# Optimization experiments

Hardware: AMD Instinct MI355X
Metric: run time of the kernel (lower is better)

The kernel has to match this reference:

```python
import jax, jax.numpy as jnp
import numpy as np

B, H, W, C = 4, 64, 64, 128  # input feature map; num_heads == filters == C


def setup_inputs() -> dict:
    key = jax.random.key(0)
    ks = jax.random.split(key, 5)
    x = jax.random.normal(ks[0], (B, H, W, C), dtype=jnp.float32)
    scale = 0.02  # keep QK^T logits in a sane range for softmax
    Wf = jax.random.normal(ks[1], (C, C), dtype=jnp.float32) * scale
    Wg = jax.random.normal(ks[2], (C, C), dtype=jnp.float32) * scale
    Wh = jax.random.normal(ks[3], (C, C), dtype=jnp.float32) * scale
    Wv = jax.random.normal(ks[4], (C, C), dtype=jnp.float32) * scale
    zeros = jnp.zeros((C,), dtype=jnp.float32)
    return {
        "x": x,
        "Wf": Wf, "bf": zeros,
        "Wg": Wg, "bg": zeros,
        "Wh": Wh, "bh": zeros,
        "Wv": Wv, "bv": zeros,
        "gamma": jnp.float32(0.01),
    }


def reference(x, Wf, bf, Wg, bg, Wh, bh, Wv, bv, gamma):
    b, h, w, c = x.shape
    n = h * w
    xf = x.reshape(b, n, c)  # 1x1 conv == per-pixel linear
    f = xf @ Wf + bf  # [b, n, heads]
    g = xf @ Wg + bg
    v = xf @ Wh + bh
    # full spatial self-attention, unscaled logits (as in the original)
    s = jnp.einsum("bnc,bmc->bnm", f, g)  # [b, n, n]
    att = jax.nn.softmax(s, axis=-1)
    ctx = jnp.einsum("bnm,bmc->bnc", att, v)  # [b, n, heads]
    ctx = gamma * ctx
    # 1x1 conv v (linear activation) + residual
    o = ctx @ Wv + bv + xf
    return o.reshape(b, h, w, -1)
```

## Files before the change

kernel.cpp:

```cpp
#include <hip/hip_runtime.h>
#include <hip/hip_bf16.h>


typedef __hip_bfloat16 bf16;
typedef float  floatx4 __attribute__((ext_vector_type(4)));
typedef short  shortx8 __attribute__((ext_vector_type(8)));
typedef short  shortx4 __attribute__((ext_vector_type(4)));

#define CDIM 128
#define NROW 16384
#define NPB  4096
#define LDW  136
#define LDK  72
#define NSPLIT 4
#define KT   16
#define QTILE 128

__device__ __forceinline__ short f2bf(float v) {
    union { __hip_bfloat16 h; short s; } u; u.h = __float2bfloat16(v); return u.s;
}
__device__ __forceinline__ float bf2f(short s) {
    union { short s2; __hip_bfloat16 h; } u; u.s2 = s; return __bfloat162float(u.h);
}

__global__ __launch_bounds__(256) void proj3_kernel(
    const float* __restrict__ x,
    const float* __restrict__ Wf, const float* __restrict__ bf_,
    const float* __restrict__ Wg, const float* __restrict__ bg_,
    const float* __restrict__ Wh, const float* __restrict__ bh_,
    bf16* __restrict__ f, bf16* __restrict__ g, bf16* __restrict__ vT)
{
    __shared__ bf16 wt[128 * LDW];

    const int t    = threadIdx.x;
    const int wave = t >> 6, lane = t & 63;
    const int quad = lane >> 4, l16 = lane & 15;
    const int mtx    = blockIdx.x >> 8;
    const int rowblk = (blockIdx.x & 255) * 64;
    const int row    = rowblk + wave * 16 + l16;

    const float* Ws[3] = {Wf, Wg, Wh};
    const float* Bs[3] = {bf_, bg_, bh_};
    const float* W    = Ws[mtx];
    const float* bias = Bs[mtx];

    for (int i = t; i < 128 * 32; i += 256) {
        int k = i >> 5, n0 = (i & 31) * 4;
        floatx4 wv = *(const floatx4*)(W + k * CDIM + n0);
#pragma unroll
        for (int j = 0; j < 4; ++j)
            *(short*)&wt[(n0 + j) * LDW + k] = f2bf(wv[j]);
    }

    shortx8 afr[4];
    {
        const float* xp = x + (size_t)row * CDIM + quad * 8;
#pragma unroll
        for (int kc = 0; kc < 4; ++kc) {
            floatx4 u = *(const floatx4*)(xp + kc * 32);
            floatx4 w = *(const floatx4*)(xp + kc * 32 + 4);
            shortx8 a;
            a[0]=f2bf(u[0]); a[1]=f2bf(u[1]); a[2]=f2bf(u[2]); a[3]=f2bf(u[3]);
            a[4]=f2bf(w[0]); a[5]=f2bf(w[1]); a[6]=f2bf(w[2]); a[7]=f2bf(w[3]);
            afr[kc] = a;
        }
    }
    __syncthreads();

    floatx4 acc[8];
#pragma unroll
    for (int nt = 0; nt < 8; ++nt) acc[nt] = (floatx4){0.f, 0.f, 0.f, 0.f};
#pragma unroll
    for (int nt = 0; nt < 8; ++nt) {
        const bf16* wrow = &wt[(nt * 16 + l16) * LDW + quad * 8];
#pragma unroll
        for (int kc = 0; kc < 4; ++kc) {
            shortx8 b = *(const shortx8*)(wrow + kc * 32);
            acc[nt] = __builtin_amdgcn_mfma_f32_16x16x32_bf16(afr[kc], b, acc[nt], 0, 0, 0);
        }
    }

    if (mtx < 2) {
        bf16* dst = (mtx == 0) ? f : g;
#pragma unroll
        for (int nt = 0; nt < 8; ++nt) {
            int col = nt * 16 + l16;
            float bv_ = bias[col];
#pragma unroll
            for (int r = 0; r < 4; ++r) {
                int orow = rowblk + wave * 16 + quad * 4 + r;
                *(short*)&dst[(size_t)orow * CDIM + col] = f2bf(acc[nt][r] + bv_);
            }
        }
    } else {
        __syncthreads();
        bf16* vt = wt;
        const int nloc0 = wave * 16 + quad * 4;
#pragma unroll
        for (int nt = 0; nt < 8; ++nt) {
            int ch = nt * 16 + l16;
            float bv_ = bias[ch];
            shortx4 pk;
#pragma unroll
            for (int r = 0; r < 4; ++r) pk[r] = f2bf(acc[nt][r] + bv_);
            *(shortx4*)&vt[ch * LDK + nloc0] = pk;
        }
        __syncthreads();
        const int ch  = t >> 1;
        const int seg = (t & 1) * 32;
        const int batch = rowblk >> 12;
        const int n0 = (rowblk & 4095) + seg;
        bf16* dst = &vT[((size_t)batch * CDIM + ch) * NPB + n0];
        const bf16* src = &vt[ch * LDK + seg];
#pragma unroll
        for (int j = 0; j < 4; ++j)
            *(shortx8*)(dst + j * 8) = *(const shortx8*)(src + j * 8);
    }
}

__global__ __launch_bounds__(256, 2) void attn_kernel(
    const bf16* __restrict__ f, const bf16* __restrict__ g,
    const bf16* __restrict__ vT,
    bf16* __restrict__ Opart, float* __restrict__ lbuf)
{
    __shared__ bf16 gs[64 * LDW];
    __shared__ bf16 vs[128 * LDK];
    __shared__ bf16 ps[4 * 32 * LDK];

    const int t    = threadIdx.x;
    const int wave = t >> 6, lane = t & 63;
    const int quad = lane >> 4, l16 = lane & 15;
    const int qg    = blockIdx.x;
    const int split = blockIdx.y;
    const int b  = qg >> 5;
    const int qt = qg & 31;
    const int qbase = b * NPB + qt * QTILE + wave * 32;

    shortx8 qf[2][4];
#pragma unroll
    for (int sub = 0; sub < 2; ++sub) {
        const bf16* qp = f + (size_t)(qbase + sub * 16 + l16) * CDIM + quad * 8;
#pragma unroll
        for (int kc = 0; kc < 4; ++kc) qf[sub][kc] = *(const shortx8*)(qp + kc * 32);
    }

    floatx4 o[2][8];
#pragma unroll
    for (int sub = 0; sub < 2; ++sub)
#pragma unroll
        for (int ct = 0; ct < 8; ++ct) o[sub][ct] = (floatx4){0.f, 0.f, 0.f, 0.f};
    float lacc[2][4];
#pragma unroll
    for (int sub = 0; sub < 2; ++sub)
#pragma unroll
        for (int r = 0; r < 4; ++r) lacc[sub][r] = 0.f;

    const bf16* gptr = g + (size_t)b * NPB * CDIM;
    const bf16* vptr = vT + (size_t)b * CDIM * NPB;

    const int gkey = t >> 4, gch = (t & 15) * 8;
    const int vch  = t >> 3, vk0 = (t & 7) * 8;

    shortx8 gx[4], vx[4];
    {
        const int kt = split * KT;
#pragma unroll
        for (int i = 0; i < 4; ++i) {
            gx[i] = *(const shortx8*)&gptr[(size_t)(kt * 64 + i * 16 + gkey) * CDIM + gch];
            vx[i] = *(const shortx8*)&vptr[(size_t)(i * 32 + vch) * NPB + kt * 64 + vk0];
        }
    }

    for (int it = 0; it < KT; ++it) {
        __syncthreads();
#pragma unroll
        for (int i = 0; i < 4; ++i) {
            *(shortx8*)&gs[(i * 16 + gkey) * LDW + gch] = gx[i];
            *(shortx8*)&vs[(i * 32 + vch) * LDK + vk0] = vx[i];
        }
        if (it + 1 < KT) {
            const int kt = split * KT + it + 1;
#pragma unroll
            for (int i = 0; i < 4; ++i) {
                gx[i] = *(const shortx8*)&gptr[(size_t)(kt * 64 + i * 16 + gkey) * CDIM + gch];
                vx[i] = *(const shortx8*)&vptr[(size_t)(i * 32 + vch) * NPB + kt * 64 + vk0];
            }
        }
        __syncthreads();

        floatx4 s[2][4];
#pragma unroll
        for (int sub = 0; sub < 2; ++sub)
#pragma unroll
            for (int nt = 0; nt < 4; ++nt) s[sub][nt] = (floatx4){0.f, 0.f, 0.f, 0.f};
#pragma unroll
        for (int nt = 0; nt < 4; ++nt) {
            const bf16* grow = &gs[(nt * 16 + l16) * LDW + quad * 8];
#pragma unroll
            for (int kc = 0; kc < 4; ++kc) {
                shortx8 bfr = *(const shortx8*)(grow + kc * 32);
                s[0][nt] = __builtin_amdgcn_mfma_f32_16x16x32_bf16(qf[0][kc], bfr, s[0][nt], 0, 0, 0);
                s[1][nt] = __builtin_amdgcn_mfma_f32_16x16x32_bf16(qf[1][kc], bfr, s[1][nt], 0, 0, 0);
            }
        }

#pragma unroll
        for (int sub = 0; sub < 2; ++sub) {
            bf16* pw = &ps[(wave * 32 + sub * 16 + quad * 4) * LDK];
#pragma unroll
            for (int r = 0; r < 4; ++r) {
#pragma unroll
                for (int nt = 0; nt < 4; ++nt) {
                    float p = __expf(s[sub][nt][r]);
                    *(short*)&pw[r * LDK + nt * 16 + l16] = f2bf(p);
                    lacc[sub][r] += p;
                }
            }
        }

        shortx8 pa[2][2];
#pragma unroll
        for (int sub = 0; sub < 2; ++sub) {
            const bf16* pr = &ps[(wave * 32 + sub * 16 + l16) * LDK + quad * 8];
            pa[sub][0] = *(const shortx8*)pr;
            pa[sub][1] = *(const shortx8*)(pr + 32);
        }

#pragma unroll
        for (int ct = 0; ct < 8; ++ct) {
            const bf16* vrow = &vs[(ct * 16 + l16) * LDK + quad * 8];
#pragma unroll
            for (int kc2 = 0; kc2 < 2; ++kc2) {
                shortx8 bfr = *(const shortx8*)(vrow + kc2 * 32);
                o[0][ct] = __builtin_amdgcn_mfma_f32_16x16x32_bf16(pa[0][kc2], bfr, o[0][ct], 0, 0, 0);
                o[1][ct] = __builtin_amdgcn_mfma_f32_16x16x32_bf16(pa[1][kc2], bfr, o[1][ct], 0, 0, 0);
            }
        }
    }

    const size_t pbase = ((size_t)qg * NSPLIT + split) * QTILE * CDIM;
#pragma unroll
    for (int sub = 0; sub < 2; ++sub)
#pragma unroll
        for (int ct = 0; ct < 8; ++ct) {
            int col = ct * 16 + l16;
#pragma unroll
            for (int r = 0; r < 4; ++r) {
                int rl = wave * 32 + sub * 16 + quad * 4 + r;
                *(short*)&Opart[pbase + (size_t)rl * CDIM + col] = f2bf(o[sub][ct][r]);
            }
        }
    float* lb = lbuf + ((size_t)qg * NSPLIT + split) * QTILE;
#pragma unroll
    for (int sub = 0; sub < 2; ++sub)
#pragma unroll
        for (int r = 0; r < 4; ++r) {
            float v = lacc[sub][r];
            v += __shfl_xor(v, 1);
            v += __shfl_xor(v, 2);
            v += __shfl_xor(v, 4);
            v += __shfl_xor(v, 8);
            if (l16 == 0) lb[wave * 32 + sub * 16 + quad * 4 + r] = v;
        }
}

__global__ __launch_bounds__(256) void out_kernel(
    const bf16* __restrict__ Opart, const float* __restrict__ lbuf,
    const float* __restrict__ Wv, const float* __restrict__ bv,
    const float* __restrict__ x, const float* __restrict__ gamma,
    float* __restrict__ out)
{
    __shared__ bf16 wt[128 * LDW];

    const int t    = threadIdx.x;
    const int wave = t >> 6, lane = t & 63;
    const int quad = lane >> 4, l16 = lane & 15;
    const int rowblk = blockIdx.x * 64;
    const int row    = rowblk + wave * 16 + l16;

    const float gm = gamma[0];
    for (int i = t; i < 128 * 32; i += 256) {
        int k = i >> 5, n0 = (i & 31) * 4;
        floatx4 wv4 = *(const floatx4*)(Wv + k * CDIM + n0);
#pragma unroll
        for (int j = 0; j < 4; ++j)
            *(short*)&wt[(n0 + j) * LDW + k] = f2bf(wv4[j] * gm);
    }

    const int qg = row >> 7, rl = row & 127;
    float L = 0.f;
#pragma unroll
    for (int s = 0; s < NSPLIT; ++s)
        L += lbuf[((size_t)qg * NSPLIT + s) * QTILE + rl];
    const float inv = 1.0f / L;

    shortx8 afr[4];
#pragma unroll
    for (int kc = 0; kc < 4; ++kc) {
        float a8[8] = {0,0,0,0,0,0,0,0};
#pragma unroll
        for (int s = 0; s < NSPLIT; ++s) {
            const bf16* p = &Opart[(((size_t)qg * NSPLIT + s) * QTILE + rl) * CDIM + quad * 8 + kc * 32];
            shortx8 v = *(const shortx8*)p;
#pragma unroll
            for (int j = 0; j < 8; ++j) a8[j] += bf2f(v[j]);
        }
        shortx8 a;
#pragma unroll
        for (int j = 0; j < 8; ++j) a[j] = f2bf(a8[j] * inv);
        afr[kc] = a;
    }
    __syncthreads();

    floatx4 acc[8];
#pragma unroll
    for (int nt = 0; nt < 8; ++nt) acc[nt] = (floatx4){0.f, 0.f, 0.f, 0.f};
#pragma unroll
    for (int nt = 0; nt < 8; ++nt) {
        const bf16* wrow = &wt[(nt * 16 + l16) * LDW + quad * 8];
#pragma unroll
        for (int kc = 0; kc < 4; ++kc) {
            shortx8 b = *(const shortx8*)(wrow + kc * 32);
            acc[nt] = __builtin_amdgcn_mfma_f32_16x16x32_bf16(afr[kc], b, acc[nt], 0, 0, 0);
        }
    }

#pragma unroll
    for (int nt = 0; nt < 8; ++nt) {
        int col = nt * 16 + l16;
        float bias = bv[col];
#pragma unroll
        for (int r = 0; r < 4; ++r) {
            int orow = rowblk + wave * 16 + quad * 4 + r;
            size_t idx = (size_t)orow * CDIM + col;
            out[idx] = acc[nt][r] + bias + x[idx];
        }
    }
}

extern "C" void kernel_launch(void* const* d_in, const int* in_sizes, int n_in,
                              void* d_out, int out_size, void* d_ws, size_t ws_size,
                              hipStream_t stream)
{
    const float* x   = (const float*)d_in[0];
    const float* Wf  = (const float*)d_in[1];
    const float* bf_ = (const float*)d_in[2];
    const float* Wg  = (const float*)d_in[3];
    const float* bg_ = (const float*)d_in[4];
    const float* Wh  = (const float*)d_in[5];
    const float* bh_ = (const float*)d_in[6];
    const float* Wv  = (const float*)d_in[7];
    const float* bv  = (const float*)d_in[8];
    const float* gm  = (const float*)d_in[9];
    float* out = (float*)d_out;

    bf16* f     = (bf16*)d_ws;
    bf16* g     = f + (size_t)NROW * CDIM;
    bf16* vT    = g + (size_t)NROW * CDIM;
    bf16* Opart = vT + (size_t)4 * CDIM * NPB;
    float* lbuf = (float*)(Opart + (size_t)128 * NSPLIT * QTILE * CDIM);

    proj3_kernel<<<768, 256, 0, stream>>>(x, Wf, bf_, Wg, bg_, Wh, bh_, f, g, vT);
    attn_kernel<<<dim3(128, NSPLIT), 256, 0, stream>>>(f, g, vT, Opart, lbuf);
    out_kernel<<<256, 256, 0, stream>>>(Opart, lbuf, Wv, bv, x, gm, out);
}
```

Measured before the change: 151.7 us.

## Double attention query tile to 256 rows and make key split count runtime

The attention kernel now runs 512-thread blocks, each covering 256 queries. Every G/V tile loaded into shared memory is therefore reused by twice as many waves, and each thread issues half as many global loads per tile. The MFMA operands are swapped so that each lane holds a contiguous row of P and O. This allows packed 4-element stores to shared memory and to the partial output, and reduces the row-sum to two shuffles. The key split becomes a runtime choice (8 when the workspace is large enough, else 4); the tradeoff is higher register and LDS pressure per block under launch_bounds(512,4).

```diff
diff --git a/kernel.cpp b/kernel.cpp
--- a/kernel.cpp
+++ b/kernel.cpp
@@ -12,9 +12,8 @@
 #define NPB  4096
 #define LDW  136
 #define LDK  72
-#define NSPLIT 4
-#define KT   16
-#define QTILE 128
+#define LDP  72
+#define QTILE 256
 
 __device__ __forceinline__ short f2bf(float v) {
     union { __hip_bfloat16 h; short s; } u; u.h = __float2bfloat16(v); return u.s;
@@ -118,22 +117,23 @@
     }
 }
 
-__global__ __launch_bounds__(256, 2) void attn_kernel(
+__global__ __launch_bounds__(512, 4) void attn_kernel(
     const bf16* __restrict__ f, const bf16* __restrict__ g,
     const bf16* __restrict__ vT,
-    bf16* __restrict__ Opart, float* __restrict__ lbuf)
+    bf16* __restrict__ Opart, float* __restrict__ lbuf,
+    int nsplit, int ktps)
 {
     __shared__ bf16 gs[64 * LDW];
     __shared__ bf16 vs[128 * LDK];
-    __shared__ bf16 ps[4 * 32 * LDK];
+    __shared__ bf16 ps[QTILE * LDP];
 
     const int t    = threadIdx.x;
     const int wave = t >> 6, lane = t & 63;
     const int quad = lane >> 4, l16 = lane & 15;
     const int qg    = blockIdx.x;
     const int split = blockIdx.y;
-    const int b  = qg >> 5;
-    const int qt = qg & 31;
+    const int b  = qg >> 4;
+    const int qt = qg & 15;
     const int qbase = b * NPB + qt * QTILE + wave * 32;
 
     shortx8 qf[2][4];
@@ -149,11 +149,7 @@
     for (int sub = 0; sub < 2; ++sub)
 #pragma unroll
         for (int ct = 0; ct < 8; ++ct) o[sub][ct] = (floatx4){0.f, 0.f, 0.f, 0.f};
-    float lacc[2][4];
-#pragma unroll
-    for (int sub = 0; sub < 2; ++sub)
-#pragma unroll
-        for (int r = 0; r < 4; ++r) lacc[sub][r] = 0.f;
+    float lacc[2] = {0.f, 0.f};
 
     const bf16* gptr = g + (size_t)b * NPB * CDIM;
     const bf16* vptr = vT + (size_t)b * CDIM * NPB;
@@ -161,29 +157,29 @@
     const int gkey = t >> 4, gch = (t & 15) * 8;
     const int vch  = t >> 3, vk0 = (t & 7) * 8;
 
-    shortx8 gx[4], vx[4];
+    shortx8 gx[2], vx[2];
     {
-        const int kt = split * KT;
-#pragma unroll
-        for (int i = 0; i < 4; ++i) {
-            gx[i] = *(const shortx8*)&gptr[(size_t)(kt * 64 + i * 16 + gkey) * CDIM + gch];
-            vx[i] = *(const shortx8*)&vptr[(size_t)(i * 32 + vch) * NPB + kt * 64 + vk0];
-        }
-    }
-
-    for (int it = 0; it < KT; ++it) {
+        const int kt = split * ktps;
+#pragma unroll
+        for (int i = 0; i < 2; ++i) {
+            gx[i] = *(const shortx8*)&gptr[(size_t)(kt * 64 + i * 32 + gkey) * CDIM + gch];
+            vx[i] = *(const shortx8*)&vptr[(size_t)(i * 64 + vch) * NPB + kt * 64 + vk0];
+        }
+    }
+
+    for (int it = 0; it < ktps; ++it) {
         __syncthreads();
 #pragma unroll
-        for (int i = 0; i < 4; ++i) {
-            *(shortx8*)&gs[(i * 16 + gkey) * LDW + gch] = gx[i];
-            *(shortx8*)&vs[(i * 32 + vch) * LDK + vk0] = vx[i];
-        }
-        if (it + 1 < KT) {
-            const int kt = split * KT + it + 1;
-#pragma unroll
-            for (int i = 0; i < 4; ++i) {
-                gx[i] = *(const shortx8*)&gptr[(size_t)(kt * 64 + i * 16 + gkey) * CDIM + gch];
-                vx[i] = *(const shortx8*)&vptr[(size_t)(i * 32 + vch) * NPB + kt * 64 + vk0];
+        for (int i = 0; i < 2; ++i) {
+            *(shortx8*)&gs[(i * 32 + gkey) * LDW + gch] = gx[i];
+            *(shortx8*)&vs[(i * 64 + vch) * LDK + vk0] = vx[i];
+        }
+        if (it + 1 < ktps) {
+            const int kt = split * ktps + it + 1;
+#pragma unroll
+            for (int i = 0; i < 2; ++i) {
+                gx[i] = *(const shortx8*)&gptr[(size_t)(kt * 64 + i * 32 + gkey) * CDIM + gch];
+                vx[i] = *(const shortx8*)&vptr[(size_t)(i * 64 + vch) * NPB + kt * 64 + vk0];
             }
         }
         __syncthreads();
@@ -198,30 +194,34 @@
             const bf16* grow = &gs[(nt * 16 + l16) * LDW + quad * 8];
 #pragma unroll
             for (int kc = 0; kc < 4; ++kc) {
-                shortx8 bfr = *(const shortx8*)(grow + kc * 32);
-                s[0][nt] = __builtin_amdgcn_mfma_f32_16x16x32_bf16(qf[0][kc], bfr, s[0][nt], 0, 0, 0);
-                s[1][nt] = __builtin_amdgcn_mfma_f32_16x16x32_bf16(qf[1][kc], bfr, s[1][nt], 0, 0, 0);
+                shortx8 gfr = *(const shortx8*)(grow + kc * 32);
+                s[0][nt] = __builtin_amdgcn_mfma_f32_16x16x32_bf16(gfr, qf[0][kc], s[0][nt], 0, 0, 0);
+                s[1][nt] = __builtin_amdgcn_mfma_f32_16x16x32_bf16(gfr, qf[1][kc], s[1][nt], 0, 0, 0);
             }
         }
 
 #pragma unroll
         for (int sub = 0; sub < 2; ++sub) {
-            bf16* pw = &ps[(wave * 32 + sub * 16 + quad * 4) * LDK];
-#pragma unroll
-            for (int r = 0; r < 4; ++r) {
-#pragma unroll
-                for (int nt = 0; nt < 4; ++nt) {
+            bf16* pw = &ps[(wave * 32 + sub * 16 + l16) * LDP];
+#pragma unroll
+            for (int nt = 0; nt < 4; ++nt) {
+                shortx4 pk;
+                float ls = 0.f;
+#pragma unroll
+                for (int r = 0; r < 4; ++r) {
                     float p = __expf(s[sub][nt][r]);
-                    *(short*)&pw[r * LDK + nt * 16 + l16] = f2bf(p);
-                    lacc[sub][r] += p;
+                    pk[r] = f2bf(p);
+                    ls += p;
                 }
+                *(shortx4*)&pw[nt * 16 + quad * 4] = pk;
+                lacc[sub] += ls;
             }
         }
 
         shortx8 pa[2][2];
 #pragma unroll
         for (int sub = 0; sub < 2; ++sub) {
-            const bf16* pr = &ps[(wave * 32 + sub * 16 + l16) * LDK + quad * 8];
+            const bf16* pr = &ps[(wave * 32 + sub * 16 + l16) * LDP + quad * 8];
             pa[sub][0] = *(const shortx8*)pr;
             pa[sub][1] = *(const shortx8*)(pr + 32);
         }
@@ -231,44 +231,40 @@
             const bf16* vrow = &vs[(ct * 16 + l16) * LDK + quad * 8];
 #pragma unroll
             for (int kc2 = 0; kc2 < 2; ++kc2) {
-                shortx8 bfr = *(const shortx8*)(vrow + kc2 * 32);
-                o[0][ct] = __builtin_amdgcn_mfma_f32_16x16x32_bf16(pa[0][kc2], bfr, o[0][ct], 0, 0, 0);
-                o[1][ct] = __builtin_amdgcn_mfma_f32_16x16x32_bf16(pa[1][kc2], bfr, o[1][ct], 0, 0, 0);
-            }
-        }
-    }
-
-    const size_t pbase = ((size_t)qg * NSPLIT + split) * QTILE * CDIM;
-#pragma unroll
-    for (int sub = 0; sub < 2; ++sub)
+                shortx8 vfr = *(const shortx8*)(vrow + kc2 * 32);
+                o[0][ct] = __builtin_amdgcn_mfma_f32_16x16x32_bf16(vfr, pa[0][kc2], o[0][ct], 0, 0, 0);
+                o[1][ct] = __builtin_amdgcn_mfma_f32_16x16x32_bf16(vfr, pa[1][kc2], o[1][ct], 0, 0, 0);
+            }
+        }
+    }
+
+    const size_t pbase = ((size_t)qg * nsplit + split) * QTILE * CDIM;
+#pragma unroll
+    for (int sub = 0; sub < 2; ++sub) {
+        const int q = wave * 32 + sub * 16 + l16;
 #pragma unroll
         for (int ct = 0; ct < 8; ++ct) {
-            int col = ct * 16 + l16;
-#pragma unroll
-            for (int r = 0; r < 4; ++r) {
-                int rl = wave * 32 + sub * 16 + quad * 4 + r;
-                *(short*)&Opart[pbase + (size_t)rl * CDIM + col] = f2bf(o[sub][ct][r]);
-            }
-        }
-    float* lb = lbuf + ((size_t)qg * NSPLIT + split) * QTILE;
-#pragma unroll
-    for (int sub = 0; sub < 2; ++sub)
-#pragma unroll
-        for (int r = 0; r < 4; ++r) {
-            float v = lacc[sub][r];
-            v += __shfl_xor(v, 1);
-            v += __shfl_xor(v, 2);
-            v += __shfl_xor(v, 4);
-            v += __shfl_xor(v, 8);
-            if (l16 == 0) lb[wave * 32 + sub * 16 + quad * 4 + r] = v;
-        }
+            shortx4 pk;
+#pragma unroll
+            for (int r = 0; r < 4; ++r) pk[r] = f2bf(o[sub][ct][r]);
+            *(shortx4*)&Opart[pbase + (size_t)q * CDIM + ct * 16 + quad * 4] = pk;
+        }
+    }
+    float* lb = lbuf + ((size_t)qg * nsplit + split) * QTILE;
+#pragma unroll
+    for (int sub = 0; sub < 2; ++sub) {
+        float v = lacc[sub];
+        v += __shfl_xor(v, 16);
+        v += __shfl_xor(v, 32);
+        if (quad == 0) lb[wave * 32 + sub * 16 + l16] = v;
+    }
 }
 
 __global__ __launch_bounds__(256) void out_kernel(
     const bf16* __restrict__ Opart, const float* __restrict__ lbuf,
     const float* __restrict__ Wv, const float* __restrict__ bv,
     const float* __restrict__ x, const float* __restrict__ gamma,
-    float* __restrict__ out)
+    float* __restrict__ out, int nsplit)
 {
     __shared__ bf16 wt[128 * LDW];
 
@@ -287,20 +283,18 @@
             *(short*)&wt[(n0 + j) * LDW + k] = f2bf(wv4[j] * gm);
     }
 
-    const int qg = row >> 7, rl = row & 127;
+    const int qg = row >> 8, rl = row & 255;
     float L = 0.f;
-#pragma unroll
-    for (int s = 0; s < NSPLIT; ++s)
-        L += lbuf[((size_t)qg * NSPLIT + s) * QTILE + rl];
+    for (int s = 0; s < nsplit; ++s)
+        L += lbuf[((size_t)qg * nsplit + s) * QTILE + rl];
     const float inv = 1.0f / L;
 
     shortx8 afr[4];
 #pragma unroll
     for (int kc = 0; kc < 4; ++kc) {
         float a8[8] = {0,0,0,0,0,0,0,0};
-#pragma unroll
-        for (int s = 0; s < NSPLIT; ++s) {
-            const bf16* p = &Opart[(((size_t)qg * NSPLIT + s) * QTILE + rl) * CDIM + quad * 8 + kc * 32];
+        for (int s = 0; s < nsplit; ++s) {
+            const bf16* p = &Opart[(((size_t)qg * nsplit + s) * QTILE + rl) * CDIM + quad * 8 + kc * 32];
             shortx8 v = *(const shortx8*)p;
 #pragma unroll
             for (int j = 0; j < 8; ++j) a8[j] += bf2f(v[j]);
@@ -354,13 +348,20 @@
     const float* gm  = (const float*)d_in[9];
     float* out = (float*)d_out;
 
+    const size_t fgv_el = (size_t)3 * NROW * CDIM;
+    size_t need8 = (fgv_el + (size_t)64 * 8 * QTILE * CDIM) * 2
+
+                 + (size_t)64 * 8 * QTILE * 4;
+    const int nsplit = (ws_size >= need8) ? 8 : 4;
+    const int ktps   = 64 / nsplit;
+
     bf16* f     = (bf16*)d_ws;
     bf16* g     = f + (size_t)NROW * CDIM;
     bf16* vT    = g + (size_t)NROW * CDIM;
     bf16* Opart = vT + (size_t)4 * CDIM * NPB;
-    float* lbuf = (float*)(Opart + (size_t)128 * NSPLIT * QTILE * CDIM);
+    float* lbuf = (float*)(Opart + (size_t)64 * nsplit * QTILE * CDIM);
 
     proj3_kernel<<<768, 256, 0, stream>>>(x, Wf, bf_, Wg, bg_, Wh, bh_, f, g, vT);
-    attn_kernel<<<dim3(128, NSPLIT), 256, 0, stream>>>(f, g, vT, Opart, lbuf);
-    out_kernel<<<256, 256, 0, stream>>>(Opart, lbuf, Wv, bv, x, gm, out);
-}
+    attn_kernel<<<dim3(64, nsplit), 512, 0, stream>>>(f, g, vT, Opart, lbuf, nsplit, ktps);
+    out_kernel<<<256, 256, 0, stream>>>(Opart, lbuf, Wv, bv, x, gm, out, nsplit);
+}
```

Measured after the change: 261.7 us. 72.5% more time.
